# Performance work log

Hardware: AMD Instinct MI355X
Metric: run time of the kernel (lower is better)

Reference implementation:

```python
import jax, jax.numpy as jnp
import numpy as np

B, T, D, H = 2, 1024, 1024, 16
WINDOW = 32
KSZ = 2 * WINDOW + 1
MAXG = 32


def setup_inputs() -> dict:
    key = jax.random.key(0)
    ks = jax.random.split(key, 5)
    s = 0.02
    x = jax.random.normal(ks[0], (B, T, D), jnp.float32)
    Wq = jax.random.normal(ks[1], (D, D), jnp.float32) * s
    Wk = jax.random.normal(ks[2], (D, D), jnp.float32) * s
    Wv = jax.random.normal(ks[3], (D, D), jnp.float32) * s
    Wo = jax.random.normal(ks[4], (D, D), jnp.float32) * s
    # global tokens: one every T//MAXG positions (same for every batch row)
    global_mask = jnp.tile((jnp.arange(T) % (T // MAXG) == 0)[None, :], (B, 1))
    return {"x": x, "global_mask": global_mask, "Wq": Wq, "Wk": Wk,
            "Wv": Wv, "Wo": Wo, "maxG": MAXG}


def reference(x, global_mask, Wq, Wk, Wv, Wo, maxG):
    Bb, Tt, Dm = x.shape
    dh = Dm // H
    scale = dh ** -0.5

    def proj(W):
        return (x @ W.T).reshape(Bb, Tt, H, dh).transpose(0, 2, 1, 3)  # (B,H,T,dh)

    q, k, v = proj(Wq), proj(Wk), proj(Wv)

    # sliding windows via zero-padded gather (== F.unfold with padding=WINDOW)
    widx = jnp.arange(Tt)[:, None] + jnp.arange(KSZ)[None, :]  # index into padded axis

    def windows(t):
        tp = jnp.pad(t, ((0, 0), (0, 0), (WINDOW, WINDOW), (0, 0)))
        return tp[:, :, widx, :]  # (B,H,T,KSZ,dh)

    Kw, Vw = windows(k), windows(v)
    scores_local = jnp.einsum('bhtd,bhtwd->bhtw', q, Kw) * scale

    # pack global-token indices (stable argsort puts True positions first, in order)
    order = jnp.argsort(jnp.logical_not(global_mask), axis=1, stable=True)
    gidx = order[:, :maxG]                                   # (B,maxG)
    gvalid = jnp.take_along_axis(global_mask, gidx, axis=1)  # (B,maxG) bool
    gather_b = jax.vmap(lambda arr, i: arr[:, i, :])         # (H,T,dh),(maxG,)->(H,maxG,dh)
    Kg = gather_b(k, gidx) * gvalid[:, None, :, None]
    Vg = gather_b(v, gidx) * gvalid[:, None, :, None]

    scores_global = jnp.einsum('bhtd,bhgd->bhtg', q, Kg) * scale
    scores_global = jnp.where(gvalid[:, None, None, :], scores_global, -1e9)

    attn = jax.nn.softmax(jnp.concatenate([scores_local, scores_global], axis=-1), axis=-1)
    wl, wg = attn[..., :KSZ], attn[..., KSZ:]
    ctx = (jnp.einsum('bhtw,bhtwd->bhtd', wl, Vw)
           + jnp.einsum('bhtg,bhgd->bhtd', wg, Vg))
    out = ctx.transpose(0, 2, 1, 3).reshape(Bb, Tt, Dm) @ Wo.T

    # ---- debug full attention map (vectorized replica of the per-token loop) ----
    t = jnp.arange(Tt)
    left = jnp.maximum(0, t - WINDOW)
    win_len = jnp.minimum(Tt, t + WINDOW + 1) - left           # (T,)
    valid_w = jnp.arange(KSZ)[None, :] < win_len[:, None]      # (T,KSZ)
    s_loc = jnp.where(valid_w[None, None], scores_local, -jnp.inf)
    attn_d = jax.nn.softmax(jnp.concatenate([s_loc, scores_global], axis=-1), axis=-1)
    wl_d = attn_d[..., :KSZ] * valid_w[None, None]             # (B,H,T,KSZ)
    wg_d = attn_d[..., KSZ:] * gvalid[:, None, None, :]        # (B,H,T,maxG)
    cols = jnp.minimum(left[:, None] + jnp.arange(KSZ)[None, :], Tt - 1)  # (T,KSZ)
    rows = jnp.broadcast_to(t[:, None], (Tt, KSZ))
    full_attn = jnp.zeros((Bb, H, Tt, Tt), x.dtype)
    full_attn = full_attn.at[:, :, rows, cols].add(wl_d)
    full_attn = jax.vmap(lambda fa, w, gi: fa.at[:, :, gi].add(w))(full_attn, wg_d, gidx)
    return out, full_attn
```

## Files before the change

### kernel.cpp

```cpp
#include <hip/hip_runtime.h>

#define T_   1024
#define B_   2
#define H_   16
#define DH   64
#define D_   1024
#define WND  32
#define KSZ  65
#define NG   32

typedef float f32x4 __attribute__((ext_vector_type(4)));
typedef __bf16 bf16x8 __attribute__((ext_vector_type(8)));
typedef __bf16 bf16x4 __attribute__((ext_vector_type(4)));
typedef unsigned short u16x4 __attribute__((ext_vector_type(4)));

__device__ __forceinline__ unsigned short f2bf(float f) {
  unsigned u = __float_as_uint(f);
  return (unsigned short)((u + 0x7fffu + ((u >> 16) & 1u)) >> 16);
}

__device__ __forceinline__ void gload16(const unsigned short* g, unsigned short* l) {
  __builtin_amdgcn_global_load_lds(
      (const __attribute__((address_space(1))) unsigned int*)g,
      (__attribute__((address_space(3))) unsigned int*)l, 16, 0, 0);
}

#define SFIDX(r, c) ((r) * 128 + ((c) ^ (((r) & 7) << 3)))

__global__ __launch_bounds__(256) void cvt_kernel(const float* __restrict__ x,
    const float* __restrict__ wq, const float* __restrict__ wk,
    const float* __restrict__ wv, const float* __restrict__ wo,
    unsigned short* __restrict__ dst,
    const int* __restrict__ mask, int* __restrict__ gidxo, float* __restrict__ gvalo) {
  if (blockIdx.x == 6144) {
    if (threadIdx.x < 128) {
      int b = threadIdx.x >> 6, lane = threadIdx.x & 63;
      const int* mb = mask + b * T_;
      unsigned long long lanemask = (1ull << lane) - 1ull;
      int base = 0;
      for (int c = 0; c < 16 && base < NG; ++c) {
        int t = c * 64 + lane;
        bool m = mb[t] != 0;
        unsigned long long bal = __ballot(m);
        int rank = __popcll(bal & lanemask);
        if (m && base + rank < NG) { gidxo[b*NG+base+rank] = t; gvalo[b*NG+base+rank] = 1.f; }
        base += __popcll(bal);
      }
      if (base < NG) {
        for (int c = 0; c < 16 && base < NG; ++c) {
          int t = c * 64 + lane;
          bool m = mb[t] == 0;
          unsigned long long bal = __ballot(m);
          int rank = __popcll(bal & lanemask);
          if (m && base + rank < NG) { gidxo[b*NG+base+rank] = t; gvalo[b*NG+base+rank] = 0.f; }
          base += __popcll(bal);
        }
      }
    }
    return;
  }
  int idx = (blockIdx.x * 256 + threadIdx.x) * 4;
  int r = idx >> 20;
  const float* src; int off;
  if (r < 2)       { src = x;  off = idx; }
  else if (r == 2) { src = wq; off = idx - 2 * 1048576; }
  else if (r == 3) { src = wk; off = idx - 3 * 1048576; }
  else if (r == 4) { src = wv; off = idx - 4 * 1048576; }
  else             { src = wo; off = idx - 5 * 1048576; }
  f32x4 v = *(const f32x4*)(src + off);
  u16x4 o;
  o.x = f2bf(v[0]); o.y = f2bf(v[1]); o.z = f2bf(v[2]); o.w = f2bf(v[3]);
  *(u16x4*)(dst + idx) = o;
}

template<int BM, int BK>
__global__ __launch_bounds__(256) void gemm128(const unsigned short* __restrict__ A,
    const unsigned short* __restrict__ B0, const unsigned short* __restrict__ B1,
    const unsigned short* __restrict__ B2,
    void* __restrict__ C0v, void* __restrict__ C1v, void* __restrict__ C2v) {
  constexpr int K = 1024;
  constexpr int FM = BM / 32;
  constexpr int WM = BM / 2;
  constexpr int CPR = BK / 8;
  constexpr int AIT = BM * CPR / 256;
  constexpr int BIT = 128 * CPR / 256;
  __shared__ __attribute__((aligned(16))) unsigned short SMEM[BM * BK + 128 * BK];
  unsigned short* As = SMEM;
  unsigned short* Bs = SMEM + BM * BK;

  int m0 = blockIdx.x * BM, n0 = blockIdx.y * 128;
  int zz = blockIdx.z;
  const unsigned short* Bb = (zz == 0 ? B0 : (zz == 1 ? B1 : B2));

  int tid = threadIdx.x;
  int w = tid >> 6, l = tid & 63;
  int wr = w >> 1, wc = w & 1;
  int lr = l & 15, kg = l >> 4;

  f32x4 acc[FM][4] = {};

  for (int kt = 0; kt < K; kt += BK) {
    __syncthreads();
#pragma unroll
    for (int i = 0; i < AIT; ++i) {
      int ci = tid + 256 * i;
      int row = ci / CPR, c8 = (ci % CPR) ^ (row & 7);
      gload16(A + (size_t)(m0 + row) * K + kt + c8 * 8, As + ci * 8);
    }
#pragma unroll
    for (int i = 0; i < BIT; ++i) {
      int ci = tid + 256 * i;
      int row = ci / CPR, c8 = (ci % CPR) ^ (row & 7);
      gload16(Bb + (size_t)(n0 + row) * K + kt + c8 * 8, Bs + ci * 8);
    }
    __syncthreads();
#pragma unroll
    for (int kk = 0; kk < BK / 32; ++kk) {
      int c8 = kk * 4 + kg;
      bf16x8 af[FM], bfr[4];
#pragma unroll
      for (int mi = 0; mi < FM; ++mi) {
        int row = wr * WM + mi * 16 + lr;
        af[mi] = *(bf16x8*)&As[row * BK + (((c8 ^ (row & 7))) * 8)];
      }
#pragma unroll
      for (int ni = 0; ni < 4; ++ni) {
        int row = wc * 64 + ni * 16 + lr;
        bfr[ni] = *(bf16x8*)&Bs[row * BK + (((c8 ^ (row & 7))) * 8)];
      }
#pragma unroll
      for (int mi = 0; mi < FM; ++mi)
#pragma unroll
        for (int ni = 0; ni < 4; ++ni)
          acc[mi][ni] = __builtin_amdgcn_mfma_f32_16x16x32_bf16(af[mi], bfr[ni], acc[mi][ni], 0, 0, 0);
    }
  }

  if (zz < 2) {
    unsigned short* C = (unsigned short*)(zz == 0 ? C0v : C1v);
#pragma unroll
    for (int mi = 0; mi < FM; ++mi)
#pragma unroll
      for (int ni = 0; ni < 4; ++ni) {
        int mbase = m0 + wr * WM + mi * 16 + (l >> 4) * 4;
        int n = n0 + wc * 64 + ni * 16 + lr;
#pragma unroll
        for (int r = 0; r < 4; ++r) {
          __bf16 v = (__bf16)acc[mi][ni][r];
          C[(size_t)(mbase + r) * 1024 + n] = *(unsigned short*)&v;
        }
      }
  } else {
    constexpr int RS = BM * 2;
    constexpr int TCH = BM / 8;
    constexpr int NIT = 128 * TCH / 256;
    __syncthreads();
    char* Tb = (char*)SMEM;
#pragma unroll
    for (int mi = 0; mi < FM; ++mi)
#pragma unroll
      for (int ni = 0; ni < 4; ++ni) {
        int mb2 = wr * WM + mi * 16 + (l >> 4) * 4;
        int nl = wc * 64 + ni * 16 + lr;
        bf16x4 pk;
        pk[0] = (__bf16)acc[mi][ni][0]; pk[1] = (__bf16)acc[mi][ni][1];
        pk[2] = (__bf16)acc[mi][ni][2]; pk[3] = (__bf16)acc[mi][ni][3];
        *(bf16x4*)(Tb + ((nl * RS + mb2 * 2) ^ ((nl & 7) << 4))) = pk;
      }
    __syncthreads();
    unsigned short* C = (unsigned short*)C2v;
    int bb = m0 >> 10, tbase = m0 & 1023;
#pragma unroll
    for (int it = 0; it < NIT; ++it) {
      int ci = tid + 256 * it;
      int dl = ci / TCH, tc = ci % TCH;
      bf16x8 v = *(bf16x8*)(Tb + ((dl * RS + tc * 16) ^ ((dl & 7) << 4)));
      int n = n0 + dl, hh = n >> 6, dd = n & 63;
      *(bf16x8*)&C[((size_t)(bb * H_ + hh) * DH + dd) * T_ + tbase + tc * 8] = v;
    }
  }
}

__global__ __launch_bounds__(256) void out_gemm(const unsigned short* __restrict__ A,
    const unsigned short* __restrict__ Bw, float* __restrict__ C) {
  constexpr int K = 1024;
  __shared__ __attribute__((aligned(16))) unsigned short SMEM[64 * 64 * 2];
  unsigned short* As = SMEM;
  unsigned short* Bs = SMEM + 64 * 64;

  int m0 = blockIdx.x * 64, n0 = blockIdx.y * 64;
  int tid = threadIdx.x;
  int w = tid >> 6, l = tid & 63;
  int wr = w >> 1, wc = w & 1;
  int lr = l & 15, kg = l >> 4;

  f32x4 acc[2][2] = {};

  for (int kt = 0; kt < K; kt += 64) {
    __syncthreads();
#pragma unroll
    for (int i = 0; i < 2; ++i) {
      int ci = tid + 256 * i;
      int row = ci >> 3, c8 = (ci & 7) ^ (row & 7);
      gload16(A + (size_t)(m0 + row) * K + kt + c8 * 8, As + ci * 8);
    }
#pragma unroll
    for (int i = 0; i < 2; ++i) {
      int ci = tid + 256 * i;
      int row = ci >> 3, c8 = (ci & 7) ^ (row & 7);
      gload16(Bw + (size_t)(n0 + row) * K + kt + c8 * 8, Bs + ci * 8);
    }
    __syncthreads();
#pragma unroll
    for (int kk = 0; kk < 2; ++kk) {
      int c8 = kk * 4 + kg;
      bf16x8 af[2], bfr[2];
#pragma unroll
      for (int mi = 0; mi < 2; ++mi) {
        int row = wr * 32 + mi * 16 + lr;
        af[mi] = *(bf16x8*)&As[row * 64 + ((c8 ^ (row & 7)) * 8)];
      }
#pragma unroll
      for (int ni = 0; ni < 2; ++ni) {
        int row = wc * 32 + ni * 16 + lr;
        bfr[ni] = *(bf16x8*)&Bs[row * 64 + ((c8 ^ (row & 7)) * 8)];
      }
#pragma unroll
      for (int mi = 0; mi < 2; ++mi)
#pragma unroll
        for (int ni = 0; ni < 2; ++ni)
          acc[mi][ni] = __builtin_amdgcn_mfma_f32_16x16x32_bf16(af[mi], bfr[ni], acc[mi][ni], 0, 0, 0);
    }
  }

#pragma unroll
  for (int mi = 0; mi < 2; ++mi)
#pragma unroll
    for (int ni = 0; ni < 2; ++ni) {
      int mbase = m0 + wr * 32 + mi * 16 + (l >> 4) * 4;
      int n = n0 + wc * 32 + ni * 16 + lr;
#pragma unroll
      for (int r = 0; r < 4; ++r)
        C[(size_t)(mbase + r) * 1024 + n] = acc[mi][ni][r];
    }
}

__global__ __launch_bounds__(512, 6) void attn_kernel(
    const unsigned short* __restrict__ qg, const unsigned short* __restrict__ kg_,
    const unsigned short* __restrict__ vg,
    const int* __restrict__ gidx_g, const float* __restrict__ gval_g,
    unsigned short* __restrict__ ctxb, float* __restrict__ fa) {
  int tid = threadIdx.x;
  int lid = blockIdx.x + 32 * blockIdx.y + 512 * blockIdx.z;
  int swz = (lid & 7) * 128 + (lid >> 3);
  int b = swz >> 9, h = (swz >> 5) & 15;
  int t0 = (swz & 31) * 32;
  int lane = tid & 63, wv = tid >> 6;

  __shared__ __attribute__((aligned(16))) unsigned short QbL[32 * 64];
  __shared__ __attribute__((aligned(16))) unsigned short KbL[128 * 64];
  __shared__ __attribute__((aligned(16))) unsigned short VtL[64 * 128];
  __shared__ __attribute__((aligned(16))) unsigned short WbL[32 * 128];
  __shared__ float m_out_s[32], invdo_s[32], rowfac_s[32];
  __shared__ int   gidx_s[32];
  __shared__ float gval_s[32];
  float* Sfp = (float*)KbL;

  if (tid < 32) { gidx_s[tid] = gidx_g[b * NG + tid]; gval_s[tid] = gval_g[b * NG + tid]; }
  ((unsigned long long*)WbL)[tid] = 0ull;
  ((unsigned long long*)WbL)[tid + 512] = 0ull;
  __syncthreads();

  const unsigned short* qbh = qg + (size_t)(b * T_ + t0) * D_ + h * DH;
  const unsigned short* kbh = kg_ + (size_t)(b * T_) * D_ + h * DH;
  const unsigned short* vbh = vg + (size_t)(b * H_ + h) * DH * T_;

  if (tid < 256) {
    int r = tid >> 3, c8 = tid & 7;
    bf16x8 v = *(const bf16x8*)(qbh + (size_t)r * D_ + c8 * 8);
    *(bf16x8*)((char*)QbL + ((r * 128 + c8 * 16) ^ ((r & 7) << 4))) = v;
  }
#pragma unroll
  for (int it = 0; it < 2; ++it) {
    int fi = tid + it * 512;
    int r = fi >> 3, c8 = fi & 7;
    int col; bool valid;
    if (r < 96) { col = t0 - 32 + r; valid = (col >= 0 && col < T_); }
    else { int g = r - 96; valid = gval_s[g] > 0.f; col = valid ? gidx_s[g] : 0; }
    bf16x8 v = {};
    if (valid) v = *(const bf16x8*)(kbh + (size_t)col * D_ + c8 * 8);
    *(bf16x8*)((char*)KbL + ((r * 128 + c8 * 16) ^ ((r & 7) << 4))) = v;
  }
#pragma unroll
  for (int it = 0; it < 2; ++it) {
    int fi = tid + it * 512;
    if (fi < 768) {
      int d = fi / 12, rc = fi % 12;
      int cb = t0 - 32 + rc * 8;
      bf16x8 v = {};
      if (cb >= 0 && cb < T_) v = *(const bf16x8*)(vbh + d * T_ + cb);
      *(bf16x8*)((char*)VtL + ((d * 256 + rc * 16) ^ ((d & 7) << 4))) = v;
    }
  }
#pragma unroll
  for (int it = 0; it < 4; ++it) {
    int fi = tid + it * 512;
    int d = fi >> 5, g = fi & 31;
    unsigned short v = 0;
    if (gval_s[g] > 0.f) v = vbh[d * T_ + gidx_s[g]];
    *(unsigned short*)((char*)VtL + ((d * 256 + (96 + g) * 2) ^ ((d & 7) << 4))) = v;
  }
  __syncthreads();

  {
    int mt = wv & 1, nq = wv >> 1;
    int lrr = lane & 15, kgl = lane >> 4;
    int arow = mt * 16 + lrr;
    f32x4 acc0 = {}, acc1 = {};
#pragma unroll
    for (int s = 0; s < 2; ++s) {
      int c = s * 4 + kgl;
      bf16x8 a = *(bf16x8*)((char*)QbL + ((arow * 128 + c * 16) ^ ((arow & 7) << 4)));
      int br0 = nq * 32 + lrr, br1 = nq * 32 + 16 + lrr;
      bf16x8 b0 = *(bf16x8*)((char*)KbL + ((br0 * 128 + c * 16) ^ ((br0 & 7) << 4)));
      bf16x8 b1 = *(bf16x8*)((char*)KbL + ((br1 * 128 + c * 16) ^ ((br1 & 7) << 4)));
      acc0 = __builtin_amdgcn_mfma_f32_16x16x32_bf16(a, b0, acc0, 0, 0, 0);
      acc1 = __builtin_amdgcn_mfma_f32_16x16x32_bf16(a, b1, acc1, 0, 0, 0);
    }
    __syncthreads();
    int orow = mt * 16 + (lane >> 4) * 4;
#pragma unroll
    for (int i = 0; i < 4; ++i) {
      Sfp[SFIDX(orow + i, nq * 32 + lrr)] = acc0[i] * 0.125f;
      Sfp[SFIDX(orow + i, nq * 32 + 16 + lrr)] = acc1[i] * 0.125f;
    }
  }
  __syncthreads();

  {
    int r = tid >> 4, lg = tid & 15;
    int t_abs = t0 + r;
    int left = (t_abs - WND > 0) ? (t_abs - WND) : 0;
    int tmp = t_abs + WND + 1; if (tmp > T_) tmp = T_;
    int wl = tmp - left;
    float sv[8]; bool vld[8], vdd[8];
#pragma unroll
    for (int ii = 0; ii < 8; ++ii) {
      int c = lg + ii * 16;
      bool loc = (c >= r && c <= r + 64);
      bool glob = (c >= 96);
      float s = Sfp[SFIDX(r, c)];
      if (glob && !(gval_s[c - 96] > 0.f)) s = -1e9f;
      vld[ii] = loc || glob;
      vdd[ii] = loc ? ((c - r) < wl) : glob;
      sv[ii] = s;
    }
    float mo = -1e30f, md = -1e30f;
#pragma unroll
    for (int ii = 0; ii < 8; ++ii) {
      if (vld[ii]) mo = fmaxf(mo, sv[ii]);
      if (vdd[ii]) md = fmaxf(md, sv[ii]);
    }
#pragma unroll
    for (int o = 1; o < 16; o <<= 1) {
      mo = fmaxf(mo, __shfl_xor(mo, o, 16));
      md = fmaxf(md, __shfl_xor(md, o, 16));
    }
    float eo = 0.f, ed = 0.f;
#pragma unroll
    for (int ii = 0; ii < 8; ++ii) {
      if (vld[ii]) eo += __expf(sv[ii] - mo);
      if (vdd[ii]) ed += __expf(sv[ii] - md);
    }
#pragma unroll
    for (int o = 1; o < 16; o <<= 1) {
      eo += __shfl_xor(eo, o, 16);
      ed += __shfl_xor(ed, o, 16);
    }
    if (lg == 0) {
      m_out_s[r] = mo;
      invdo_s[r] = 1.f / eo;
      rowfac_s[r] = (eo / ed) * __expf(mo - md);
    }
  }
  __syncthreads();

  for (int idx = tid; idx < 32 * 97; idx += 512) {
    int t = idx / 97;
    int j = idx - t * 97;
    int cc = (j < KSZ) ? (t + j) : (j + 31);
    float s = Sfp[SFIDX(t, cc)];
    float wgt = __expf(s - m_out_s[t]) * invdo_s[t];
    Sfp[SFIDX(t, cc)] = wgt;
    *(unsigned short*)((char*)WbL + ((t * 256 + cc * 2) ^ ((t & 7) << 4))) = f2bf(wgt);
  }
  __syncthreads();

  {
    int mt = wv >> 1, nt = wv & 1;
    int lrr = lane & 15, kgl = lane >> 4;
    int arow = mt * 16 + lrr;
    int brow = nt * 16 + lrr;
    f32x4 acc = {};
#pragma unroll
    for (int s = 0; s < 4; ++s) {
      int c = s * 4 + kgl;
      bf16x8 a = *(bf16x8*)((char*)VtL + ((arow * 256 + c * 16) ^ ((arow & 7) << 4)));
      bf16x8 bb = *(bf16x8*)((char*)WbL + ((brow * 256 + c * 16) ^ ((brow & 7) << 4)));
      acc = __builtin_amdgcn_mfma_f32_16x16x32_bf16(a, bb, acc, 0, 0, 0);
    }
    int t = nt * 16 + lrr;
    int dbase = mt * 16 + (lane >> 4) * 4;
    u16x4 st;
    st.x = f2bf(acc[0]); st.y = f2bf(acc[1]); st.z = f2bf(acc[2]); st.w = f2bf(acc[3]);
    *(u16x4*)(ctxb + ((size_t)(b * T_ + t0 + t)) * D_ + h * DH + dbase) = st;
  }

  {
    int rp = tid >> 8;
    int c0 = (tid & 255) * 4;
    unsigned gm = 0;
#pragma unroll
    for (int g = 0; g < NG; ++g) {
      int gc = gidx_s[g];
      if (gval_s[g] > 0.f && gc >= c0 && gc < c0 + 4) gm |= (1u << g);
    }
#pragma unroll 2
    for (int rr = 0; rr < 16; ++rr) {
      int r = rr * 2 + rp;
      int t_abs = t0 + r;
      int left = (t_abs - WND > 0) ? (t_abs - WND) : 0;
      int tmp = t_abs + WND + 1; if (tmp > T_) tmp = T_;
      int wl = tmp - left;
      float rf = rowfac_s[r];
      f32x4 o = {0.f, 0.f, 0.f, 0.f};
      int jj0 = c0 - left;
      if (jj0 > -4 && jj0 < wl) {
#pragma unroll
        for (int e = 0; e < 4; ++e) {
          int jj = jj0 + e;
          if (jj >= 0 && jj < wl) o[e] = Sfp[SFIDX(r, r + jj)] * rf;
        }
      }
      if (gm) {
        unsigned mm = gm;
        while (mm) {
          int g = __ffs(mm) - 1; mm &= mm - 1;
          o[gidx_s[g] - c0] += Sfp[SFIDX(r, 96 + g)] * rf;
        }
      }
      float* dst = fa + (((size_t)(b * H_ + h) * T_) + t_abs) * T_ + c0;
      *(f32x4*)dst = o;
    }
  }
}

extern "C" void kernel_launch(void* const* d_in, const int* in_sizes, int n_in,
                              void* d_out, int out_size, void* d_ws, size_t ws_size,
                              hipStream_t stream) {
  const float* x   = (const float*)d_in[0];
  const int* gmask = (const int*)d_in[1];
  const float* wq  = (const float*)d_in[2];
  const float* wk  = (const float*)d_in[3];
  const float* wv  = (const float*)d_in[4];
  const float* wo  = (const float*)d_in[5];

  unsigned short* arena = (unsigned short*)d_ws;
  unsigned short* xb  = arena;
  unsigned short* wqb = arena + 2 * 1048576;
  unsigned short* wkb = arena + 3 * 1048576;
  unsigned short* wvb = arena + 4 * 1048576;
  unsigned short* wob = arena + 5 * 1048576;
  unsigned short* qb   = arena + 6 * 1048576;
  unsigned short* kb   = arena + 8 * 1048576;
  unsigned short* vtb  = arena + 10 * 1048576;
  unsigned short* ctxb = arena + 12 * 1048576;
  int*   gidx = (int*)(arena + 14 * 1048576);
  float* gval = (float*)(gidx + 64);

  float* outp = (float*)d_out;
  float* fa   = outp + 2097152;

  cvt_kernel<<<dim3(6145), dim3(256), 0, stream>>>(x, wq, wk, wv, wo, xb, gmask, gidx, gval);
  gemm128<64, 128><<<dim3(32, 8, 3), dim3(256), 0, stream>>>(xb, wqb, wkb, wvb, qb, kb, vtb);
  attn_kernel<<<dim3(32, 16, 2), dim3(512), 0, stream>>>(qb, kb, vtb, gidx, gval, ctxb, fa);
  out_gemm<<<dim3(32, 16), dim3(256), 0, stream>>>(ctxb, wob, outp);
}
```

Measured before the change: 86.70 us.

## Double-buffer LDS tiles in the QKV and output GEMMs

Both GEMM kernels now hold two LDS buffers. The next K-tile is loaded asynchronously into the spare buffer while MFMAs run on the current one, which leaves one barrier per iteration instead of two. The QKV GEMM's K-tile drops from 128 to 64 so the doubled buffers fit in the same LDS footprint, at the cost of twice as many loop iterations. The redundant barrier before the transposed V epilogue is removed because the loop already ends on a barrier.

Result: faster. 81.95 us (median of 2 runs) (-5.5%).

```diff
diff --git a/kernel.cpp b/kernel.cpp
--- a/kernel.cpp
+++ b/kernel.cpp
@@ -84,9 +84,8 @@
   constexpr int CPR = BK / 8;
   constexpr int AIT = BM * CPR / 256;
   constexpr int BIT = 128 * CPR / 256;
-  __shared__ __attribute__((aligned(16))) unsigned short SMEM[BM * BK + 128 * BK];
-  unsigned short* As = SMEM;
-  unsigned short* Bs = SMEM + BM * BK;
+  constexpr int HALF = (BM + 128) * BK;
+  __shared__ __attribute__((aligned(16))) unsigned short SMEM[2 * HALF];
 
   int m0 = blockIdx.x * BM, n0 = blockIdx.y * 128;
   int zz = blockIdx.z;
@@ -99,41 +98,69 @@
 
   f32x4 acc[FM][4] = {};
 
-  for (int kt = 0; kt < K; kt += BK) {
-    __syncthreads();
+  {
+    unsigned short* As = SMEM;
+    unsigned short* Bs = SMEM + BM * BK;
 #pragma unroll
     for (int i = 0; i < AIT; ++i) {
       int ci = tid + 256 * i;
       int row = ci / CPR, c8 = (ci % CPR) ^ (row & 7);
-      gload16(A + (size_t)(m0 + row) * K + kt + c8 * 8, As + ci * 8);
+      gload16(A + (size_t)(m0 + row) * K + c8 * 8, As + ci * 8);
     }
 #pragma unroll
     for (int i = 0; i < BIT; ++i) {
       int ci = tid + 256 * i;
       int row = ci / CPR, c8 = (ci % CPR) ^ (row & 7);
-      gload16(Bb + (size_t)(n0 + row) * K + kt + c8 * 8, Bs + ci * 8);
+      gload16(Bb + (size_t)(n0 + row) * K + c8 * 8, Bs + ci * 8);
+    }
+  }
+  __syncthreads();
+
+  int cur = 0;
+  for (int kt = 0; kt < K; kt += BK) {
+    if (kt + BK < K) {
+      unsigned short* As = SMEM + (cur ^ 1) * HALF;
+      unsigned short* Bs = As + BM * BK;
+      int ktn = kt + BK;
+#pragma unroll
+      for (int i = 0; i < AIT; ++i) {
+        int ci = tid + 256 * i;
+        int row = ci / CPR, c8 = (ci % CPR) ^ (row & 7);
+        gload16(A + (size_t)(m0 + row) * K + ktn + c8 * 8, As + ci * 8);
+      }
+#pragma unroll
+      for (int i = 0; i < BIT; ++i) {
+        int ci = tid + 256 * i;
+        int row = ci / CPR, c8 = (ci % CPR) ^ (row & 7);
+        gload16(Bb + (size_t)(n0 + row) * K + ktn + c8 * 8, Bs + ci * 8);
+      }
+    }
+    {
+      unsigned short* As = SMEM + cur * HALF;
+      unsigned short* Bs = As + BM * BK;
+#pragma unroll
+      for (int kk = 0; kk < BK / 32; ++kk) {
+        int c8 = kk * 4 + kg;
+        bf16x8 af[FM], bfr[4];
+#pragma unroll
+        for (int mi = 0; mi < FM; ++mi) {
+          int row = wr * WM + mi * 16 + lr;
+          af[mi] = *(bf16x8*)&As[row * BK + ((c8 ^ (row & 7)) * 8)];
+        }
+#pragma unroll
+        for (int ni = 0; ni < 4; ++ni) {
+          int row = wc * 64 + ni * 16 + lr;
+          bfr[ni] = *(bf16x8*)&Bs[row * BK + ((c8 ^ (row & 7)) * 8)];
+        }
+#pragma unroll
+        for (int mi = 0; mi < FM; ++mi)
+#pragma unroll
+          for (int ni = 0; ni < 4; ++ni)
+            acc[mi][ni] = __builtin_amdgcn_mfma_f32_16x16x32_bf16(af[mi], bfr[ni], acc[mi][ni], 0, 0, 0);
+      }
     }
     __syncthreads();
-#pragma unroll
-    for (int kk = 0; kk < BK / 32; ++kk) {
-      int c8 = kk * 4 + kg;
-      bf16x8 af[FM], bfr[4];
-#pragma unroll
-      for (int mi = 0; mi < FM; ++mi) {
-        int row = wr * WM + mi * 16 + lr;
-        af[mi] = *(bf16x8*)&As[row * BK + (((c8 ^ (row & 7))) * 8)];
-      }
-#pragma unroll
-      for (int ni = 0; ni < 4; ++ni) {
-        int row = wc * 64 + ni * 16 + lr;
-        bfr[ni] = *(bf16x8*)&Bs[row * BK + (((c8 ^ (row & 7))) * 8)];
-      }
-#pragma unroll
-      for (int mi = 0; mi < FM; ++mi)
-#pragma unroll
-        for (int ni = 0; ni < 4; ++ni)
-          acc[mi][ni] = __builtin_amdgcn_mfma_f32_16x16x32_bf16(af[mi], bfr[ni], acc[mi][ni], 0, 0, 0);
-    }
+    cur ^= 1;
   }
 
   if (zz < 2) {
@@ -154,7 +181,6 @@
     constexpr int RS = BM * 2;
     constexpr int TCH = BM / 8;
     constexpr int NIT = 128 * TCH / 256;
-    __syncthreads();
     char* Tb = (char*)SMEM;
 #pragma unroll
     for (int mi = 0; mi < FM; ++mi)
@@ -184,9 +210,8 @@
 __global__ __launch_bounds__(256) void out_gemm(const unsigned short* __restrict__ A,
     const unsigned short* __restrict__ Bw, float* __restrict__ C) {
   constexpr int K = 1024;
-  __shared__ __attribute__((aligned(16))) unsigned short SMEM[64 * 64 * 2];
-  unsigned short* As = SMEM;
-  unsigned short* Bs = SMEM + 64 * 64;
+  constexpr int HALF = 128 * 64;
+  __shared__ __attribute__((aligned(16))) unsigned short SMEM[2 * HALF];
 
   int m0 = blockIdx.x * 64, n0 = blockIdx.y * 64;
   int tid = threadIdx.x;
@@ -196,41 +221,59 @@
 
   f32x4 acc[2][2] = {};
 
-  for (int kt = 0; kt < K; kt += 64) {
-    __syncthreads();
+  {
+    unsigned short* As = SMEM;
+    unsigned short* Bs = SMEM + 64 * 64;
 #pragma unroll
     for (int i = 0; i < 2; ++i) {
       int ci = tid + 256 * i;
       int row = ci >> 3, c8 = (ci & 7) ^ (row & 7);
-      gload16(A + (size_t)(m0 + row) * K + kt + c8 * 8, As + ci * 8);
-    }
-#pragma unroll
-    for (int i = 0; i < 2; ++i) {
-      int ci = tid + 256 * i;
-      int row = ci >> 3, c8 = (ci & 7) ^ (row & 7);
-      gload16(Bw + (size_t)(n0 + row) * K + kt + c8 * 8, Bs + ci * 8);
+      gload16(A + (size_t)(m0 + row) * K + c8 * 8, As + ci * 8);
+      gload16(Bw + (size_t)(n0 + row) * K + c8 * 8, Bs + ci * 8);
+    }
+  }
+  __syncthreads();
+
+  int cur = 0;
+  for (int kt = 0; kt < K; kt += 64) {
+    if (kt + 64 < K) {
+      unsigned short* As = SMEM + (cur ^ 1) * HALF;
+      unsigned short* Bs = As + 64 * 64;
+      int ktn = kt + 64;
+#pragma unroll
+      for (int i = 0; i < 2; ++i) {
+        int ci = tid + 256 * i;
+        int row = ci >> 3, c8 = (ci & 7) ^ (row & 7);
+        gload16(A + (size_t)(m0 + row) * K + ktn + c8 * 8, As + ci * 8);
+        gload16(Bw + (size_t)(n0 + row) * K + ktn + c8 * 8, Bs + ci * 8);
+      }
+    }
+    {
+      unsigned short* As = SMEM + cur * HALF;
+      unsigned short* Bs = As + 64 * 64;
+#pragma unroll
+      for (int kk = 0; kk < 2; ++kk) {
+        int c8 = kk * 4 + kg;
+        bf16x8 af[2], bfr[2];
+#pragma unroll
+        for (int mi = 0; mi < 2; ++mi) {
+          int row = wr * 32 + mi * 16 + lr;
+          af[mi] = *(bf16x8*)&As[row * 64 + ((c8 ^ (row & 7)) * 8)];
+        }
+#pragma unroll
+        for (int ni = 0; ni < 2; ++ni) {
+          int row = wc * 32 + ni * 16 + lr;
+          bfr[ni] = *(bf16x8*)&Bs[row * 64 + ((c8 ^ (row & 7)) * 8)];
+        }
+#pragma unroll
+        for (int mi = 0; mi < 2; ++mi)
+#pragma unroll
+          for (int ni = 0; ni < 2; ++ni)
+            acc[mi][ni] = __builtin_amdgcn_mfma_f32_16x16x32_bf16(af[mi], bfr[ni], acc[mi][ni], 0, 0, 0);
+      }
     }
     __syncthreads();
-#pragma unroll
-    for (int kk = 0; kk < 2; ++kk) {
-      int c8 = kk * 4 + kg;
-      bf16x8 af[2], bfr[2];
-#pragma unroll
-      for (int mi = 0; mi < 2; ++mi) {
-        int row = wr * 32 + mi * 16 + lr;
-        af[mi] = *(bf16x8*)&As[row * 64 + ((c8 ^ (row & 7)) * 8)];
-      }
-#pragma unroll
-      for (int ni = 0; ni < 2; ++ni) {
-        int row = wc * 32 + ni * 16 + lr;
-        bfr[ni] = *(bf16x8*)&Bs[row * 64 + ((c8 ^ (row & 7)) * 8)];
-      }
-#pragma unroll
-      for (int mi = 0; mi < 2; ++mi)
-#pragma unroll
-        for (int ni = 0; ni < 2; ++ni)
-          acc[mi][ni] = __builtin_amdgcn_mfma_f32_16x16x32_bf16(af[mi], bfr[ni], acc[mi][ni], 0, 0, 0);
-    }
+    cur ^= 1;
   }
 
 #pragma unroll
@@ -482,7 +525,7 @@
   float* fa   = outp + 2097152;
 
   cvt_kernel<<<dim3(6145), dim3(256), 0, stream>>>(x, wq, wk, wv, wo, xb, gmask, gidx, gval);
-  gemm128<64, 128><<<dim3(32, 8, 3), dim3(256), 0, stream>>>(xb, wqb, wkb, wvb, qb, kb, vtb);
+  gemm128<64, 64><<<dim3(32, 8, 3), dim3(256), 0, stream>>>(xb, wqb, wkb, wvb, qb, kb, vtb);
   attn_kernel<<<dim3(32, 16, 2), dim3(512), 0, stream>>>(qb, kb, vtb, gidx, gval, ctxb, fa);
   out_gemm<<<dim3(32, 16), dim3(256), 0, stream>>>(ctxb, wob, outp);
 }
```
